# Performance work log

Hardware: AMD Instinct MI355X
Metric: run time of the kernel (lower is better)

The kernel has to match this reference:

```python
import jax, jax.numpy as jnp
import numpy as np

N_NODES = 100000
N_EDGES = 1600000
IN_FEATS = 512
OUT_FEATS = 128


def setup_inputs() -> dict:
    key = jax.random.key(0)
    k1, k2, k3, k4, k5 = jax.random.split(key, 5)
    feat = jax.random.normal(k1, (N_NODES, IN_FEATS), dtype=jnp.float32)
    src = jax.random.randint(k2, (N_EDGES,), 0, N_NODES, dtype=jnp.int32)
    dst = jax.random.randint(k3, (N_EDGES,), 0, N_NODES, dtype=jnp.int32)
    edge_weight = jax.random.uniform(k4, (N_EDGES,), dtype=jnp.float32)
    # xavier_uniform init for the [in, out] weight
    limit = float(np.sqrt(6.0 / (IN_FEATS + OUT_FEATS)))
    weight = jax.random.uniform(k5, (IN_FEATS, OUT_FEATS), dtype=jnp.float32,
                                minval=-limit, maxval=limit)
    bias = jnp.zeros((OUT_FEATS,), dtype=jnp.float32)
    return {"feat": feat, "weight": weight, "bias": bias,
            "edge_weight": edge_weight, "src": src, "dst": dst}


def reference(feat, weight, bias, edge_weight, src, dst):
    n = feat.shape[0]
    ones = jnp.ones_like(edge_weight)
    # degrees from edge list; clamp(min=1)
    out_deg = jnp.maximum(jax.ops.segment_sum(ones, src, num_segments=n), 1.0)
    in_deg = jnp.maximum(jax.ops.segment_sum(ones, dst, num_segments=n), 1.0)
    # norm='both': left-normalize source feats by out_deg^-0.5
    feat_src = feat * jax.lax.rsqrt(out_deg)[:, None]
    # in_feats > out_feats -> project before aggregation
    h = feat_src @ weight                      # [N, OUT]
    msg = h[src] * edge_weight[:, None]        # u_mul_e, [E, OUT]
    rst = jax.ops.segment_sum(msg, dst, num_segments=n)  # fn.sum per dst
    # right-normalize by in_deg^-0.5, add bias (activation is None)
    rst = rst * jax.lax.rsqrt(in_deg)[:, None] + bias
    return rst
```

## Files before the change

### kernel.cpp

```cpp
#include <hip/hip_runtime.h>
#include <hip/hip_bf16.h>

#define NNODES 100000
#define NEDGES 1600000
#define INF 512
#define OUTF 128
#define NB 391
#define BCAP 5120
#define SEG 2048
#define NBUCKBLK ((NEDGES + SEG - 1) / SEG)
#define NGEMMBLK ((NNODES + 63) / 64)
#define BK 32
#define NKSTEP (INF / BK)

typedef __attribute__((ext_vector_type(8))) __bf16 bf16x8;
typedef __attribute__((ext_vector_type(4))) float f32x4;

typedef const __attribute__((address_space(1))) unsigned int* gas_ptr;
typedef __attribute__((address_space(3))) unsigned int* las_ptr;

__device__ __forceinline__ void gload_lds16(const void* g, void* l) {
  __builtin_amdgcn_global_load_lds((gas_ptr)g, (las_ptr)l, 16, 0, 0);
}

__global__ void wt_kernel(const float* __restrict__ w, unsigned short* __restrict__ wta) {
  int i = blockIdx.x * blockDim.x + threadIdx.x;
  if (i >= 8192) return;
  int lane = i & 63;
  int c8   = (i >> 6) & 7;
  int kb   = i >> 9;
  int n = c8 * 16 + (lane & 15);
  int kbase = kb * 32 + (lane >> 4) * 8;
  unsigned short tmp[8];
#pragma unroll
  for (int j = 0; j < 8; ++j) {
    __bf16 b = (__bf16)(w[(size_t)(kbase + j) * OUTF + n]);
    tmp[j] = __builtin_bit_cast(unsigned short, b);
  }
  ((int4*)wta)[i] = *(int4*)tmp;
}

struct GemmSmem { float As[2][64 * BK]; unsigned short Bs[2][4096]; };
struct BuckSmem { int hist[NB]; int base[NB]; };
union FusedSmem { GemmSmem g; BuckSmem bu; };

__global__ __launch_bounds__(256, 4) void fused_kernel(
    const float* __restrict__ feat, const unsigned short* __restrict__ wta,
    const int* __restrict__ src, const int* __restrict__ dst,
    const float* __restrict__ ew, int* __restrict__ out_cnt,
    int* __restrict__ bucket_cnt, int2* __restrict__ bucket,
    unsigned short* __restrict__ h) {
  __shared__ FusedSmem sm;
  const int t = threadIdx.x;

  if (blockIdx.x < NBUCKBLK) {
    int* hist = sm.bu.hist;
    int* base = sm.bu.base;
    for (int i = t; i < NB; i += 256) hist[i] = 0;
    __syncthreads();
    int e0 = blockIdx.x * SEG;
    int e1 = min(e0 + SEG, NEDGES);
    for (int e = e0 + t; e < e1; e += 256) {
      atomicAdd(&out_cnt[src[e]], 1);
      atomicAdd(&hist[dst[e] >> 8], 1);
    }
    __syncthreads();
    for (int i = t; i < NB; i += 256) {
      int c = hist[i];
      base[i] = c ? atomicAdd(&bucket_cnt[i], c) : 0;
      hist[i] = 0;
    }
    __syncthreads();
    for (int e = e0 + t; e < e1; e += 256) {
      int d = dst[e];
      int b = d >> 8;
      int r = atomicAdd(&hist[b], 1);
      int2 en;
      en.x = ((d & 255) << 17) | src[e];
      en.y = __float_as_int(ew[e]);
      bucket[(size_t)b * BCAP + base[b] + r] = en;
    }
    return;
  }

  const int lane = t & 63;
  const int wave = t >> 6;
  const int l15 = lane & 15;
  const int lg  = lane >> 4;
  const int rowbase = (blockIdx.x - NBUCKBLK) * 64;

  const int srow_off = lane >> 3;
  const int schunk = (lane & 7) ^ srow_off;

  f32x4 acc[8];
#pragma unroll
  for (int c = 0; c < 8; ++c) acc[c] = (f32x4){0.f, 0.f, 0.f, 0.f};

#define STAGE(buf, kb)                                                         \
  {                                                                            \
    _Pragma("unroll")                                                          \
    for (int q = 0; q < 2; ++q) {                                              \
      int i = wave * 2 + q;                                                    \
      int gr = min(rowbase + i * 8 + srow_off, NNODES - 1);                    \
      const float* ga = feat + (size_t)gr * INF + (kb) * BK + schunk * 4;      \
      gload_lds16(ga, &sm.g.As[buf][i * 256]);                                 \
      const unsigned short* gb =                                               \
          wta + (size_t)(kb) * 4096 + i * 512 + lane * 8;                      \
      gload_lds16(gb, &sm.g.Bs[buf][i * 512]);                                 \
    }                                                                          \
  }

  int buf = 0;
  STAGE(0, 0);
  __syncthreads();

  for (int kb = 0; kb < NKSTEP; ++kb) {
    if (kb + 1 < NKSTEP) STAGE(buf ^ 1, kb + 1);

    bf16x8 bfr[8];
#pragma unroll
    for (int c = 0; c < 8; ++c)
      bfr[c] = *(const bf16x8*)&sm.g.Bs[buf][c * 512 + lane * 8];

    int r = wave * 16 + l15;
    int c0 = (lg * 2) ^ (l15 & 7);
    int c1 = (lg * 2 + 1) ^ (l15 & 7);
    f32x4 u = *(const f32x4*)&sm.g.As[buf][r * 32 + c0 * 4];
    f32x4 v = *(const f32x4*)&sm.g.As[buf][r * 32 + c1 * 4];
    bf16x8 a;
#pragma unroll
    for (int j = 0; j < 4; ++j) {
      a[j]     = (__bf16)u[j];
      a[j + 4] = (__bf16)v[j];
    }

#pragma unroll
    for (int c = 0; c < 8; ++c)
      acc[c] = __builtin_amdgcn_mfma_f32_16x16x32_bf16(a, bfr[c], acc[c], 0, 0, 0);

    __syncthreads();
    buf ^= 1;
  }
#undef STAGE

  int rb = rowbase + wave * 16 + lg * 4;
#pragma unroll
  for (int r = 0; r < 4; ++r) {
    int row = rb + r;
    if (row < NNODES) {
#pragma unroll
      for (int c = 0; c < 8; ++c) {
        __bf16 bv = (__bf16)acc[c][r];
        h[(size_t)row * OUTF + c * 16 + l15] = __builtin_bit_cast(unsigned short, bv);
      }
    }
  }
}

__device__ __forceinline__ float blo(unsigned int u) { return __uint_as_float(u << 16); }
__device__ __forceinline__ float bhi(unsigned int u) { return __uint_as_float(u & 0xFFFF0000u); }

__global__ __launch_bounds__(512) void agg_kernel(
    const int* __restrict__ bucket_cnt, const int2* __restrict__ bucket,
    const int* __restrict__ out_cnt, int2* __restrict__ epair,
    const unsigned short* __restrict__ h, const float* __restrict__ bias,
    float* __restrict__ out) {
  __shared__ int hist[256];
  __shared__ int rowp[256];
  __shared__ int cur[256];
  __shared__ int dcnt[256];
  const int b = blockIdx.x;
  const int t = threadIdx.x;
  const int nb = bucket_cnt[b];
  const int2* bk = bucket + (size_t)b * BCAP;
  int2* ep = epair + (size_t)b * BCAP;

  if (t < 256) hist[t] = 0;
  __syncthreads();
  for (int i = t; i < nb; i += 512) atomicAdd(&hist[bk[i].x >> 17], 1);
  __syncthreads();
  int myv = (t < 256) ? hist[t] : 0;
  __syncthreads();
  for (int off = 1; off < 256; off <<= 1) {
    int x = (t < 256 && t >= off) ? hist[t - off] : 0;
    __syncthreads();
    if (t < 256) hist[t] += x;
    __syncthreads();
  }
  if (t < 256) {
    int excl = hist[t] - myv;
    rowp[t] = excl;
    cur[t] = excl;
    dcnt[t] = myv;
  }
  __syncthreads();
  for (int i = t; i < nb; i += 512) {
    int2 en = bk[i];
    int s = en.x & 0x1FFFF;
    int nl = en.x >> 17;
    float w = __int_as_float(en.y) * rsqrtf(fmaxf((float)out_cnt[s], 1.0f));
    int r = atomicAdd(&cur[nl], 1);
    ep[r] = make_int2(s, __float_as_int(w));
  }
  __syncthreads();

  const int lane = t & 63;
  const int wv = t >> 6;
  const int half = lane >> 5;
  const int grp  = (lane >> 4) & 1;
  const int li   = lane & 15;

  for (int pi = wv; pi < 128; pi += 8) {
    const int nl = pi * 2 + half;
    const int node = b * 256 + nl;
    const int beg = rowp[nl];
    const int deg = dcnt[nl];
    const int endp = beg + deg;

    float a0 = 0.f, a1 = 0.f, a2 = 0.f, a3 = 0.f;
    float a4 = 0.f, a5 = 0.f, a6 = 0.f, a7 = 0.f;

    int e = beg + grp;
#define GSTEP(pr)                                                              \
      {                                                                        \
        const unsigned int* hp =                                               \
            (const unsigned int*)(h + (size_t)(pr).x * OUTF) + li * 4;         \
        uint4 u = *(const uint4*)hp;                                           \
        float w = __int_as_float((pr).y);                                      \
        a0 += blo(u.x) * w; a1 += bhi(u.x) * w;                                \
        a2 += blo(u.y) * w; a3 += bhi(u.y) * w;                                \
        a4 += blo(u.z) * w; a5 += bhi(u.z) * w;                                \
        a6 += blo(u.w) * w; a7 += bhi(u.w) * w;                                \
      }
    for (; e + 6 < endp; e += 8) {
      int2 p0 = ep[e];
      int2 p1 = ep[e + 2];
      int2 p2 = ep[e + 4];
      int2 p3 = ep[e + 6];
      GSTEP(p0); GSTEP(p1); GSTEP(p2); GSTEP(p3);
    }
    for (; e < endp; e += 2) {
      int2 pr = ep[e];
      GSTEP(pr);
    }
#undef GSTEP

    a0 += __shfl_xor(a0, 16); a1 += __shfl_xor(a1, 16);
    a2 += __shfl_xor(a2, 16); a3 += __shfl_xor(a3, 16);
    a4 += __shfl_xor(a4, 16); a5 += __shfl_xor(a5, 16);
    a6 += __shfl_xor(a6, 16); a7 += __shfl_xor(a7, 16);

    if (grp == 0 && node < NNODES) {
      float sc = rsqrtf(fmaxf((float)deg, 1.0f));
      f32x4 b0 = ((const f32x4*)bias)[li * 2];
      f32x4 b1 = ((const f32x4*)bias)[li * 2 + 1];
      f32x4 v0, v1;
      v0.x = a0 * sc + b0.x; v0.y = a1 * sc + b0.y;
      v0.z = a2 * sc + b0.z; v0.w = a3 * sc + b0.w;
      v1.x = a4 * sc + b1.x; v1.y = a5 * sc + b1.y;
      v1.z = a6 * sc + b1.z; v1.w = a7 * sc + b1.w;
      f32x4* op = (f32x4*)(out + (size_t)node * OUTF);
      op[li * 2] = v0;
      op[li * 2 + 1] = v1;
    }
  }
}

extern "C" void kernel_launch(void* const* d_in, const int* in_sizes, int n_in,
                              void* d_out, int out_size, void* d_ws, size_t ws_size,
                              hipStream_t stream) {
  const float* feat   = (const float*)d_in[0];
  const float* weight = (const float*)d_in[1];
  const float* bias   = (const float*)d_in[2];
  const float* ew     = (const float*)d_in[3];
  const int*   src    = (const int*)d_in[4];
  const int*   dst    = (const int*)d_in[5];
  float* out = (float*)d_out;
  char* ws = (char*)d_ws;

  int* out_cnt        = (int*)ws;
  int* bucket_cnt     = (int*)(ws + 0x100000);
  unsigned short* wta = (unsigned short*)(ws + 0x110000);
  int2* bucket        = (int2*)(ws + 0x140000);
  int2* epair         = (int2*)(ws + 0x1200000);
  unsigned short* h   = (unsigned short*)(ws + 0x2200000);

  hipMemsetAsync(out_cnt, 0, NNODES * sizeof(int), stream);
  hipMemsetAsync(bucket_cnt, 0, NB * sizeof(int), stream);

  wt_kernel<<<32, 256, 0, stream>>>(weight, wta);
  fused_kernel<<<NBUCKBLK + NGEMMBLK, 256, 0, stream>>>(feat, wta, src, dst, ew,
                                                        out_cnt, bucket_cnt, bucket, h);
  agg_kernel<<<NB, 512, 0, stream>>>(bucket_cnt, bucket, out_cnt, epair, h, bias, out);
}
```

Before: 270.2 us.

## Split fused bucket/GEMM kernel into separate sequential launches

```diff
diff --git a/kernel.cpp b/kernel.cpp
--- a/kernel.cpp
+++ b/kernel.cpp
@@ -8,8 +8,6 @@
 #define NB 391
 #define BCAP 5120
 #define SEG 2048
-#define NBUCKBLK ((NEDGES + SEG - 1) / SEG)
-#define NGEMMBLK ((NNODES + 63) / 64)
 #define BK 32
 #define NKSTEP (INF / BK)
 
@@ -40,54 +38,51 @@
   ((int4*)wta)[i] = *(int4*)tmp;
 }
 
-struct GemmSmem { float As[2][64 * BK]; unsigned short Bs[2][4096]; };
-struct BuckSmem { int hist[NB]; int base[NB]; };
-union FusedSmem { GemmSmem g; BuckSmem bu; };
-
-__global__ __launch_bounds__(256, 4) void fused_kernel(
-    const float* __restrict__ feat, const unsigned short* __restrict__ wta,
+__global__ __launch_bounds__(256) void bucket_kernel(
     const int* __restrict__ src, const int* __restrict__ dst,
     const float* __restrict__ ew, int* __restrict__ out_cnt,
-    int* __restrict__ bucket_cnt, int2* __restrict__ bucket,
+    int* __restrict__ bucket_cnt, int2* __restrict__ bucket) {
+  __shared__ int hist[NB];
+  __shared__ int base[NB];
+  int t = threadIdx.x;
+  for (int i = t; i < NB; i += 256) hist[i] = 0;
+  __syncthreads();
+  int e0 = blockIdx.x * SEG;
+  int e1 = min(e0 + SEG, NEDGES);
+  for (int e = e0 + t; e < e1; e += 256) {
+    atomicAdd(&out_cnt[src[e]], 1);
+    atomicAdd(&hist[dst[e] >> 8], 1);
+  }
+  __syncthreads();
+  for (int i = t; i < NB; i += 256) {
+    int c = hist[i];
+    base[i] = c ? atomicAdd(&bucket_cnt[i], c) : 0;
+    hist[i] = 0;
+  }
+  __syncthreads();
+  for (int e = e0 + t; e < e1; e += 256) {
+    int d = dst[e];
+    int b = d >> 8;
+    int r = atomicAdd(&hist[b], 1);
+    int2 en;
+    en.x = ((d & 255) << 17) | src[e];
+    en.y = __float_as_int(ew[e]);
+    bucket[(size_t)b * BCAP + base[b] + r] = en;
+  }
+}
+
+__global__ __launch_bounds__(256, 4) void gemm_kernel(
+    const float* __restrict__ feat, const unsigned short* __restrict__ wta,
     unsigned short* __restrict__ h) {
-  __shared__ FusedSmem sm;
+  __shared__ float As[2][64 * BK];
+  __shared__ unsigned short Bs[2][4096];
+
   const int t = threadIdx.x;
-
-  if (blockIdx.x < NBUCKBLK) {
-    int* hist = sm.bu.hist;
-    int* base = sm.bu.base;
-    for (int i = t; i < NB; i += 256) hist[i] = 0;
-    __syncthreads();
-    int e0 = blockIdx.x * SEG;
-    int e1 = min(e0 + SEG, NEDGES);
-    for (int e = e0 + t; e < e1; e += 256) {
-      atomicAdd(&out_cnt[src[e]], 1);
-      atomicAdd(&hist[dst[e] >> 8], 1);
-    }
-    __syncthreads();
-    for (int i = t; i < NB; i += 256) {
-      int c = hist[i];
-      base[i] = c ? atomicAdd(&bucket_cnt[i], c) : 0;
-      hist[i] = 0;
-    }
-    __syncthreads();
-    for (int e = e0 + t; e < e1; e += 256) {
-      int d = dst[e];
-      int b = d >> 8;
-      int r = atomicAdd(&hist[b], 1);
-      int2 en;
-      en.x = ((d & 255) << 17) | src[e];
-      en.y = __float_as_int(ew[e]);
-      bucket[(size_t)b * BCAP + base[b] + r] = en;
-    }
-    return;
-  }
-
   const int lane = t & 63;
   const int wave = t >> 6;
   const int l15 = lane & 15;
   const int lg  = lane >> 4;
-  const int rowbase = (blockIdx.x - NBUCKBLK) * 64;
+  const int rowbase = blockIdx.x * 64;
 
   const int srow_off = lane >> 3;
   const int schunk = (lane & 7) ^ srow_off;
@@ -103,10 +98,10 @@
       int i = wave * 2 + q;                                                    \
       int gr = min(rowbase + i * 8 + srow_off, NNODES - 1);                    \
       const float* ga = feat + (size_t)gr * INF + (kb) * BK + schunk * 4;      \
-      gload_lds16(ga, &sm.g.As[buf][i * 256]);                                 \
+      gload_lds16(ga, &As[buf][i * 256]);                                      \
       const unsigned short* gb =                                               \
           wta + (size_t)(kb) * 4096 + i * 512 + lane * 8;                      \
-      gload_lds16(gb, &sm.g.Bs[buf][i * 512]);                                 \
+      gload_lds16(gb, &Bs[buf][i * 512]);                                      \
     }                                                                          \
   }
 
@@ -120,13 +115,13 @@
     bf16x8 bfr[8];
 #pragma unroll
     for (int c = 0; c < 8; ++c)
-      bfr[c] = *(const bf16x8*)&sm.g.Bs[buf][c * 512 + lane * 8];
+      bfr[c] = *(const bf16x8*)&Bs[buf][c * 512 + lane * 8];
 
     int r = wave * 16 + l15;
     int c0 = (lg * 2) ^ (l15 & 7);
     int c1 = (lg * 2 + 1) ^ (l15 & 7);
-    f32x4 u = *(const f32x4*)&sm.g.As[buf][r * 32 + c0 * 4];
-    f32x4 v = *(const f32x4*)&sm.g.As[buf][r * 32 + c1 * 4];
+    f32x4 u = *(const f32x4*)&As[buf][r * 32 + c0 * 4];
+    f32x4 v = *(const f32x4*)&As[buf][r * 32 + c1 * 4];
     bf16x8 a;
 #pragma unroll
     for (int j = 0; j < 4; ++j) {
@@ -289,7 +284,8 @@
   hipMemsetAsync(bucket_cnt, 0, NB * sizeof(int), stream);
 
   wt_kernel<<<32, 256, 0, stream>>>(weight, wta);
-  fused_kernel<<<NBUCKBLK + NGEMMBLK, 256, 0, stream>>>(feat, wta, src, dst, ew,
-                                                        out_cnt, bucket_cnt, bucket, h);
+  gemm_kernel<<<(NNODES + 63) / 64, 256, 0, stream>>>(feat, wta, h);
+  bucket_kernel<<<(NEDGES + SEG - 1) / SEG, 256, 0, stream>>>(src, dst, ew, out_cnt,
+                                                              bucket_cnt, bucket);
   agg_kernel<<<NB, 512, 0, stream>>>(bucket_cnt, bucket, out_cnt, epair, h, bias, out);
 }
```

Measured after the change: 268.2 us. Within noise of the previous version (-0.7%).
